# Optimization experiments

Hardware: AMD Instinct MI355X
Metric: run time of the kernel (lower is better)

## Reference

```python
import jax, jax.numpy as jnp
import numpy as np

N_USER = 60082   # n_fields: size of station/field table
N_STATION = 14695
D = 128
B = 8
K = 32


def setup_inputs() -> dict:
    key = jax.random.key(0)
    ks = jax.random.split(key, 20)
    inp = {
        'user_embedding': jax.random.normal(ks[0], (B, D), jnp.float32),
        'station_embedding': jax.random.normal(ks[1], (N_USER, D), jnp.float32),
        'raw_field_embed': jax.random.normal(ks[2], (N_USER, D), jnp.float32),
        'his_nodes': jax.random.randint(ks[3], (B, K), 0, N_USER),
        'now_nodes': jax.random.randint(ks[4], (B, K), 0, N_USER),
        'user_id': jax.random.randint(ks[5], (B,), 0, N_STATION),
        # learned parameters
        'user_emb_table': jax.random.normal(ks[6], (N_STATION, D), jnp.float32) * 0.02,
        'station_emb_table': jax.random.normal(ks[7], (N_USER, D), jnp.float32) * 0.02,
        'proj_w': jax.random.normal(ks[8], (D, D), jnp.float32) / np.sqrt(D),
        'proj_b': jnp.zeros((D,), jnp.float32),
        'theta': jax.random.uniform(ks[9], (N_STATION, 1), jnp.float32),
        'alpha': jax.random.uniform(ks[10], (N_USER, 1), jnp.float32),
        'w_his1': jax.random.normal(ks[11], (D, D // 2), jnp.float32) / np.sqrt(D),
        'b_his1': jnp.zeros((D // 2,), jnp.float32),
        'w_his2': jax.random.normal(ks[12], (D // 2, D), jnp.float32) / np.sqrt(D // 2),
        'b_his2': jnp.zeros((D,), jnp.float32),
        'w_st': jax.random.normal(ks[13], (D, 1), jnp.float32) / np.sqrt(D),
        'b_st': jnp.zeros((1,), jnp.float32),
        'w_u': jax.random.normal(ks[14], (D, 1), jnp.float32) / np.sqrt(D),
        'b_u': jnp.zeros((1,), jnp.float32),
    }
    return inp


def reference(user_embedding, station_embedding, raw_field_embed,
              user_emb_table, station_emb_table, proj_w, proj_b,
              theta, alpha, w_his1, b_his1, w_his2, b_his2,
              w_st, b_st, w_u, b_u,
              his_nodes, now_nodes, user_id):
    # user_mem_stat: gated mix of dynamic and static user embedding (dropout = eval identity)
    th = theta[user_id]                                    # [B,1]
    user_mem = (1.0 - th) * user_embedding + th * user_emb_table[user_id]  # [B,D]

    # full-table projection, shared across batch (the torch loop recomputes it)
    proj = station_emb_table @ proj_w + proj_b             # [N,D]

    b_idx = jnp.arange(B)[:, None]                         # [B,1]
    beta = jnp.zeros((B, N_USER), user_embedding.dtype)
    beta = beta.at[b_idx, now_nodes].set(1.0)
    beta = beta.at[b_idx, his_nodes].set(1.0)              # use_his=True path

    embed = (1.0 - beta[..., None] * alpha[None]) * proj[None]  # [B,N,D]

    # scatter-add current-node contribution
    now_add = alpha[now_nodes] * station_embedding[now_nodes]  # [B,K,D]
    embed = embed.at[b_idx, now_nodes].add(now_add)

    # history MLP (Linear -> LeakyReLU -> Linear) on gathered raw field embeds
    h = raw_field_embed[his_nodes]                         # [B,K,D]
    h = jax.nn.leaky_relu(h @ w_his1 + b_his1) @ w_his2 + b_his2
    embed = embed.at[b_idx, his_nodes].add(alpha[his_nodes] * h)

    station_out = (embed @ w_st)[..., 0] + b_st[0]         # [B,N]
    user_out = user_mem @ w_u + b_u                        # [B,1]
    return station_out + user_out                          # [B,N]
```

## Files before the change

### kernel.cpp

```cpp
#include <hip/hip_runtime.h>

#define NU 60082
#define NST 14695
#define D 128
#define B 8
#define K 32

#define WS_V   0
#define WS_C   128
#define WS_UC  136
#define WS_NOW 144
#define WS_HIS 400

__global__ __launch_bounds__(256) void k_prep(
    const float* __restrict__ user_embedding,
    const float* __restrict__ station_embedding,
    const float* __restrict__ raw_field_embed,
    const int* __restrict__ his_nodes,
    const int* __restrict__ now_nodes,
    const int* __restrict__ user_id,
    const float* __restrict__ user_emb_table,
    const float* __restrict__ proj_w,
    const float* __restrict__ proj_b,
    const float* __restrict__ theta,
    const float* __restrict__ alpha,
    const float* __restrict__ w_his1,
    const float* __restrict__ b_his1,
    const float* __restrict__ w_his2,
    const float* __restrict__ b_his2,
    const float* __restrict__ w_st,
    const float* __restrict__ b_st,
    const float* __restrict__ w_u,
    const float* __restrict__ b_u,
    float* __restrict__ ws)
{
    const int t = threadIdx.x;
    if (blockIdx.x == 0) {
        if (t < 128) {
            float acc = 0.f;
            for (int j = 0; j < D; ++j) acc += proj_w[t * D + j] * w_st[j];
            ws[WS_V + t] = acc;
        } else if (t == 128) {
            float acc = 0.f;
            for (int j = 0; j < D; ++j) acc += proj_b[j] * w_st[j];
            ws[WS_C] = acc;
        } else if (t >= 136 && t < 144) {
            int b = t - 136;
            int uid = user_id[b];
            float th = theta[uid];
            float acc = 0.f;
            for (int dd = 0; dd < D; ++dd)
                acc += ((1.f - th) * user_embedding[b * D + dd] +
                        th * user_emb_table[(size_t)uid * D + dd]) * w_u[dd];
            ws[WS_UC + b] = acc + b_u[0] + b_st[0];
        }
        {
            int n = now_nodes[t];
            float acc = 0.f;
            for (int dd = 0; dd < D; ++dd)
                acc += station_embedding[(size_t)n * D + dd] * w_st[dd];
            ws[WS_NOW + t] = alpha[n] * acc;
        }
    } else {
        int wid  = (blockIdx.x - 1) * 4 + (t >> 6);
        int lane = t & 63;
        int n = his_nodes[wid];
        float v2 = 0.f, c2 = 0.f;
        for (int dd = 0; dd < D; ++dd) {
            float wst = w_st[dd];
            v2 += w_his2[lane * D + dd] * wst;
            c2 += b_his2[dd] * wst;
        }
        float h1 = b_his1[lane];
        for (int dd = 0; dd < D; ++dd)
            h1 += raw_field_embed[(size_t)n * D + dd] * w_his1[dd * 64 + lane];
        float h1a = h1 > 0.f ? h1 : 0.01f * h1;
        float contrib = h1a * v2;
        for (int off = 32; off >= 1; off >>= 1)
            contrib += __shfl_down(contrib, off, 64);
        if (lane == 0)
            ws[WS_HIS + wid] = alpha[n] * (contrib + c2);
    }
}

__global__ __launch_bounds__(256) void k_main(
    const float* __restrict__ set,
    const float* __restrict__ ws,
    float* __restrict__ out)
{
    __shared__ float s_v[128];
    __shared__ float s_tile[64];
    __shared__ float s_uc[8];
    __shared__ float s_c;
    const int t = threadIdx.x;
    if (t < 128) s_v[t] = ws[WS_V + t];
    if (t == 128) s_c = ws[WS_C];
    if (t >= 136 && t < 144) s_uc[t - 136] = ws[WS_UC + t - 136];
    __syncthreads();

    const int row0 = blockIdx.x * 64;
    const int w    = t >> 6;
    const int lane = t & 63;
    const int half = lane >> 5;
    const int l32  = lane & 31;
    const float4 vv = ((const float4*)s_v)[l32];
    const float  c  = s_c;

    for (int i = 0; i < 8; ++i) {
        int r = i * 8 + w * 2 + half;
        int row = row0 + r;
        float acc = 0.f;
        if (row < NU) {
            float4 x = ((const float4*)(set + (size_t)row * D))[l32];
            acc = x.x * vv.x + x.y * vv.y + x.z * vv.z + x.w * vv.w;
        }
        for (int off = 16; off >= 1; off >>= 1)
            acc += __shfl_down(acc, off, 32);
        if (l32 == 0) s_tile[r] = acc + c;
    }
    __syncthreads();

    const int nl = t & 63;
    const int b0 = t >> 6;
    const int row = row0 + nl;
    if (row < NU) {
        float sv = s_tile[nl];
        out[(size_t)b0 * NU + row]       = sv + s_uc[b0];
        out[(size_t)(b0 + 4) * NU + row] = sv + s_uc[b0 + 4];
    }
}

__global__ __launch_bounds__(512) void k_fix(
    const float* __restrict__ set,
    const float* __restrict__ alpha,
    const int* __restrict__ his_nodes,
    const int* __restrict__ now_nodes,
    const float* __restrict__ ws,
    float* __restrict__ out)
{
    __shared__ int   s_nodes[B][64];
    __shared__ float s_vals[B][64];
    __shared__ float s_v[128];
    __shared__ float s_c;
    const int t = threadIdx.x;
    const int b = t >> 6;
    const int j = t & 63;
    if (t < 128) s_v[t] = ws[WS_V + t];
    if (t == 128) s_c = ws[WS_C];
    if (j < K) {
        s_nodes[b][j] = now_nodes[b * K + j];
        s_vals[b][j]  = ws[WS_NOW + b * K + j];
    } else {
        s_nodes[b][j] = his_nodes[b * K + (j - K)];
        s_vals[b][j]  = ws[WS_HIS + b * K + (j - K)];
    }
    __syncthreads();
    int n = s_nodes[b][j];
    bool first = true;
    for (int i = 0; i < j; ++i)
        if (s_nodes[b][i] == n) { first = false; break; }
    if (!first) return;
    float sum = 0.f;
    for (int i = 0; i < 64; ++i)
        if (s_nodes[b][i] == n) sum += s_vals[b][i];
    float sn = s_c;
    for (int dd = 0; dd < D; ++dd)
        sn += set[(size_t)n * D + dd] * s_v[dd];
    out[(size_t)b * NU + n] = (1.f - alpha[n]) * sn + ws[WS_UC + b] + sum;
}

extern "C" void kernel_launch(void* const* d_in, const int* in_sizes, int n_in,
                              void* d_out, int out_size, void* d_ws, size_t ws_size,
                              hipStream_t stream) {
    const float* user_embedding    = (const float*)d_in[0];
    const float* station_embedding = (const float*)d_in[1];
    const float* raw_field_embed   = (const float*)d_in[2];
    const int*   his_nodes         = (const int*)d_in[3];
    const int*   now_nodes         = (const int*)d_in[4];
    const int*   user_id           = (const int*)d_in[5];
    const float* user_emb_table    = (const float*)d_in[6];
    const float* station_emb_table = (const float*)d_in[7];
    const float* proj_w            = (const float*)d_in[8];
    const float* proj_b            = (const float*)d_in[9];
    const float* theta             = (const float*)d_in[10];
    const float* alpha             = (const float*)d_in[11];
    const float* w_his1            = (const float*)d_in[12];
    const float* b_his1            = (const float*)d_in[13];
    const float* w_his2            = (const float*)d_in[14];
    const float* b_his2            = (const float*)d_in[15];
    const float* w_st              = (const float*)d_in[16];
    const float* b_st              = (const float*)d_in[17];
    const float* w_u               = (const float*)d_in[18];
    const float* b_u               = (const float*)d_in[19];
    float* out = (float*)d_out;
    float* ws  = (float*)d_ws;

    hipLaunchKernelGGL(k_prep, dim3(65), dim3(256), 0, stream,
                       user_embedding, station_embedding, raw_field_embed,
                       his_nodes, now_nodes, user_id, user_emb_table,
                       proj_w, proj_b, theta, alpha,
                       w_his1, b_his1, w_his2, b_his2,
                       w_st, b_st, w_u, b_u, ws);

    hipLaunchKernelGGL(k_main, dim3((NU + 63) / 64), dim3(256), 0, stream,
                       station_emb_table, ws, out);

    hipLaunchKernelGGL(k_fix, dim3(1), dim3(512), 0, stream,
                       station_emb_table, alpha, his_nodes, now_nodes, ws, out);
}
```

Before: 184.7 us.

## Fuse prep and fix into per-batch patch kernel, mask patched rows in main

Result: slower. 200.6 us (+8.6%).

```diff
diff --git a/kernel.cpp b/kernel.cpp
--- a/kernel.cpp
+++ b/kernel.cpp
@@ -9,10 +9,8 @@
 #define WS_V   0
 #define WS_C   128
 #define WS_UC  136
-#define WS_NOW 144
-#define WS_HIS 400
-
-__global__ __launch_bounds__(256) void k_prep(
+
+__global__ __launch_bounds__(256) void k_patch(
     const float* __restrict__ user_embedding,
     const float* __restrict__ station_embedding,
     const float* __restrict__ raw_field_embed,
@@ -20,6 +18,7 @@
     const int* __restrict__ now_nodes,
     const int* __restrict__ user_id,
     const float* __restrict__ user_emb_table,
+    const float* __restrict__ station_emb_table,
     const float* __restrict__ proj_w,
     const float* __restrict__ proj_b,
     const float* __restrict__ theta,
@@ -32,59 +31,96 @@
     const float* __restrict__ b_st,
     const float* __restrict__ w_u,
     const float* __restrict__ b_u,
-    float* __restrict__ ws)
+    float* __restrict__ ws,
+    float* __restrict__ out)
 {
+    __shared__ float s_v[128];
+    __shared__ float s_v2[64];
+    __shared__ int   s_nodes[64];
+    __shared__ float s_vals[64];
+    __shared__ float s_c, s_c2, s_uc;
     const int t = threadIdx.x;
-    if (blockIdx.x == 0) {
-        if (t < 128) {
-            float acc = 0.f;
-            for (int j = 0; j < D; ++j) acc += proj_w[t * D + j] * w_st[j];
-            ws[WS_V + t] = acc;
-        } else if (t == 128) {
-            float acc = 0.f;
-            for (int j = 0; j < D; ++j) acc += proj_b[j] * w_st[j];
-            ws[WS_C] = acc;
-        } else if (t >= 136 && t < 144) {
-            int b = t - 136;
-            int uid = user_id[b];
-            float th = theta[uid];
-            float acc = 0.f;
-            for (int dd = 0; dd < D; ++dd)
-                acc += ((1.f - th) * user_embedding[b * D + dd] +
-                        th * user_emb_table[(size_t)uid * D + dd]) * w_u[dd];
-            ws[WS_UC + b] = acc + b_u[0] + b_st[0];
-        }
-        {
-            int n = now_nodes[t];
-            float acc = 0.f;
-            for (int dd = 0; dd < D; ++dd)
-                acc += station_embedding[(size_t)n * D + dd] * w_st[dd];
-            ws[WS_NOW + t] = alpha[n] * acc;
-        }
-    } else {
-        int wid  = (blockIdx.x - 1) * 4 + (t >> 6);
-        int lane = t & 63;
-        int n = his_nodes[wid];
-        float v2 = 0.f, c2 = 0.f;
-        for (int dd = 0; dd < D; ++dd) {
-            float wst = w_st[dd];
-            v2 += w_his2[lane * D + dd] * wst;
-            c2 += b_his2[dd] * wst;
-        }
+    const int b = blockIdx.x;
+
+    if (t < 128) {
+        float acc = 0.f;
+        for (int j = 0; j < D; ++j) acc += proj_w[t * D + j] * w_st[j];
+        s_v[t] = acc;
+        if (b == 0) ws[WS_V + t] = acc;
+    } else if (t < 192) {
+        int u = t - 128;
+        float acc = 0.f;
+        for (int j = 0; j < D; ++j) acc += w_his2[u * D + j] * w_st[j];
+        s_v2[u] = acc;
+    } else if (t == 192) {
+        float acc = 0.f;
+        for (int j = 0; j < D; ++j) acc += proj_b[j] * w_st[j];
+        s_c = acc;
+        if (b == 0) ws[WS_C] = acc;
+    } else if (t == 193) {
+        float acc = 0.f;
+        for (int j = 0; j < D; ++j) acc += b_his2[j] * w_st[j];
+        s_c2 = acc;
+    } else if (t == 194) {
+        int uid = user_id[b];
+        float th = theta[uid];
+        float acc = 0.f;
+        for (int dd = 0; dd < D; ++dd)
+            acc += ((1.f - th) * user_embedding[b * D + dd] +
+                    th * user_emb_table[(size_t)uid * D + dd]) * w_u[dd];
+        float uc = acc + b_u[0] + b_st[0];
+        s_uc = uc;
+        ws[WS_UC + b] = uc;
+    }
+    if (t < 64)
+        s_nodes[t] = (t < K) ? now_nodes[b * K + t] : his_nodes[b * K + (t - K)];
+    __syncthreads();
+
+    const int w = t >> 6, lane = t & 63;
+    for (int r = 0; r < 8; ++r) {
+        int j = w * 8 + r;
+        int n = s_nodes[32 + j];
         float h1 = b_his1[lane];
         for (int dd = 0; dd < D; ++dd)
             h1 += raw_field_embed[(size_t)n * D + dd] * w_his1[dd * 64 + lane];
         float h1a = h1 > 0.f ? h1 : 0.01f * h1;
-        float contrib = h1a * v2;
+        float contrib = h1a * s_v2[lane];
         for (int off = 32; off >= 1; off >>= 1)
             contrib += __shfl_down(contrib, off, 64);
-        if (lane == 0)
-            ws[WS_HIS + wid] = alpha[n] * (contrib + c2);
+        if (lane == 0) s_vals[32 + j] = alpha[n] * (contrib + s_c2);
+    }
+    for (int r = 0; r < 8; ++r) {
+        int j = w * 8 + r;
+        int n = s_nodes[j];
+        float p = station_embedding[(size_t)n * D + lane] * w_st[lane]
+                + station_embedding[(size_t)n * D + 64 + lane] * w_st[64 + lane];
+        for (int off = 32; off >= 1; off >>= 1)
+            p += __shfl_down(p, off, 64);
+        if (lane == 0) s_vals[j] = alpha[n] * p;
+    }
+    __syncthreads();
+
+    if (t < 64) {
+        int n = s_nodes[t];
+        bool first = true;
+        for (int i = 0; i < t; ++i)
+            if (s_nodes[i] == n) { first = false; break; }
+        if (first) {
+            float sum = 0.f;
+            for (int i = 0; i < 64; ++i)
+                if (s_nodes[i] == n) sum += s_vals[i];
+            float s = s_c;
+            for (int dd = 0; dd < D; ++dd)
+                s += station_emb_table[(size_t)n * D + dd] * s_v[dd];
+            out[(size_t)b * NU + n] = (1.f - alpha[n]) * s + s_uc + sum;
+        }
     }
 }
 
 __global__ __launch_bounds__(256) void k_main(
     const float* __restrict__ set,
+    const int* __restrict__ his_nodes,
+    const int* __restrict__ now_nodes,
     const float* __restrict__ ws,
     float* __restrict__ out)
 {
@@ -92,13 +128,21 @@
     __shared__ float s_tile[64];
     __shared__ float s_uc[8];
     __shared__ float s_c;
+    __shared__ unsigned char s_flag[8 * 64];
     const int t = threadIdx.x;
-    if (t < 128) s_v[t] = ws[WS_V + t];
+    if (t < 128) { s_v[t] = ws[WS_V + t]; ((int*)s_flag)[t] = 0; }
     if (t == 128) s_c = ws[WS_C];
     if (t >= 136 && t < 144) s_uc[t - 136] = ws[WS_UC + t - 136];
     __syncthreads();
 
     const int row0 = blockIdx.x * 64;
+    {
+        int n0 = now_nodes[t];
+        if ((n0 >> 6) == (int)blockIdx.x) s_flag[(t >> 5) * 64 + (n0 & 63)] = 1;
+        int n1 = his_nodes[t];
+        if ((n1 >> 6) == (int)blockIdx.x) s_flag[(t >> 5) * 64 + (n1 & 63)] = 1;
+    }
+
     const int w    = t >> 6;
     const int lane = t & 63;
     const int half = lane >> 5;
@@ -125,48 +169,11 @@
     const int row = row0 + nl;
     if (row < NU) {
         float sv = s_tile[nl];
-        out[(size_t)b0 * NU + row]       = sv + s_uc[b0];
-        out[(size_t)(b0 + 4) * NU + row] = sv + s_uc[b0 + 4];
-    }
-}
-
-__global__ __launch_bounds__(512) void k_fix(
-    const float* __restrict__ set,
-    const float* __restrict__ alpha,
-    const int* __restrict__ his_nodes,
-    const int* __restrict__ now_nodes,
-    const float* __restrict__ ws,
-    float* __restrict__ out)
-{
-    __shared__ int   s_nodes[B][64];
-    __shared__ float s_vals[B][64];
-    __shared__ float s_v[128];
-    __shared__ float s_c;
-    const int t = threadIdx.x;
-    const int b = t >> 6;
-    const int j = t & 63;
-    if (t < 128) s_v[t] = ws[WS_V + t];
-    if (t == 128) s_c = ws[WS_C];
-    if (j < K) {
-        s_nodes[b][j] = now_nodes[b * K + j];
-        s_vals[b][j]  = ws[WS_NOW + b * K + j];
-    } else {
-        s_nodes[b][j] = his_nodes[b * K + (j - K)];
-        s_vals[b][j]  = ws[WS_HIS + b * K + (j - K)];
-    }
-    __syncthreads();
-    int n = s_nodes[b][j];
-    bool first = true;
-    for (int i = 0; i < j; ++i)
-        if (s_nodes[b][i] == n) { first = false; break; }
-    if (!first) return;
-    float sum = 0.f;
-    for (int i = 0; i < 64; ++i)
-        if (s_nodes[b][i] == n) sum += s_vals[b][i];
-    float sn = s_c;
-    for (int dd = 0; dd < D; ++dd)
-        sn += set[(size_t)n * D + dd] * s_v[dd];
-    out[(size_t)b * NU + n] = (1.f - alpha[n]) * sn + ws[WS_UC + b] + sum;
+        if (!s_flag[b0 * 64 + nl])
+            out[(size_t)b0 * NU + row] = sv + s_uc[b0];
+        if (!s_flag[(b0 + 4) * 64 + nl])
+            out[(size_t)(b0 + 4) * NU + row] = sv + s_uc[b0 + 4];
+    }
 }
 
 extern "C" void kernel_launch(void* const* d_in, const int* in_sizes, int n_in,
@@ -195,16 +202,13 @@
     float* out = (float*)d_out;
     float* ws  = (float*)d_ws;
 
-    hipLaunchKernelGGL(k_prep, dim3(65), dim3(256), 0, stream,
+    hipLaunchKernelGGL(k_patch, dim3(B), dim3(256), 0, stream,
                        user_embedding, station_embedding, raw_field_embed,
                        his_nodes, now_nodes, user_id, user_emb_table,
-                       proj_w, proj_b, theta, alpha,
+                       station_emb_table, proj_w, proj_b, theta, alpha,
                        w_his1, b_his1, w_his2, b_his2,
-                       w_st, b_st, w_u, b_u, ws);
+                       w_st, b_st, w_u, b_u, ws, out);
 
     hipLaunchKernelGGL(k_main, dim3((NU + 63) / 64), dim3(256), 0, stream,
-                       station_emb_table, ws, out);
-
-    hipLaunchKernelGGL(k_fix, dim3(1), dim3(512), 0, stream,
-                       station_emb_table, alpha, his_nodes, now_nodes, ws, out);
+                       station_emb_table, his_nodes, now_nodes, ws, out);
 }
```
